# Performance work log

Measured on AMD Instinct MI355X. Metric: run time of the kernel, lower is better.

Reference implementation:

```python
import jax, jax.numpy as jnp
import numpy as np

N_NODES = 20000
N_EDGES = 320000
D_FEAT = 256
BATCH_SIZE = 4096


def setup_inputs() -> dict:
    key = jax.random.key(0)
    k1, k2 = jax.random.split(key)
    x = jax.random.normal(k1, (N_NODES, D_FEAT), dtype=jnp.float32)
    edge_index = jax.random.randint(k2, (2, N_EDGES), 0, N_NODES, dtype=jnp.int64)
    return {"x": x, "edge_index": edge_index, "batch_size": BATCH_SIZE}


def reference(x, edge_index, batch_size):
    # SparseTensor.from_edge_index: row = edge_index[0], col = edge_index[1].
    # gcn_norm(adj, add_self_loops=False): deg[r] = row-sum (edge count per row),
    # value(r, c) = deg[r]^-0.5 * deg[c]^-0.5.
    # adj_norm.t().matmul(x): out[c] = sum_{edges (r,c)} value * x[r].
    n = x.shape[0]
    src = edge_index[0]
    dst = edge_index[1]
    deg = jax.ops.segment_sum(jnp.ones_like(src, dtype=x.dtype), src, num_segments=n)
    deg_inv_sqrt = jnp.where(deg > 0, jax.lax.rsqrt(jnp.maximum(deg, 1.0)), 0.0)
    w = deg_inv_sqrt[src] * deg_inv_sqrt[dst]  # [E]
    # Weighted gather-scatter SpMM: [E, D] gathered rows -> scatter-add to dst.
    x_neighbors_norm = jax.ops.segment_sum(x[src] * w[:, None], dst, num_segments=n)
    node_labels = jnp.concatenate([x, x_neighbors_norm], axis=-1)  # [N, 2D]
    return node_labels[:batch_size]
```

## Files before the change

kernel.cpp:

```cpp
#include <hip/hip_runtime.h>

#define D_FEAT 256
#define CAP 96

__global__ __launch_bounds__(256) void edges_kernel(
        const int* __restrict__ src, const int* __restrict__ dst,
        int n_edges, int batch,
        int* __restrict__ degi, int* __restrict__ cursor,
        int* __restrict__ novf, int* __restrict__ buckets,
        long long* __restrict__ ovf) {
    int t = blockIdx.x * blockDim.x + threadIdx.x;
    int e = t * 4;
    if (e >= n_edges) return;

    int s[4], d[4];
    int rem = n_edges - e;
    if (rem >= 4) {
        int4 s4 = *(const int4*)(src + e);
        int4 d4 = *(const int4*)(dst + e);
        s[0] = s4.x; s[1] = s4.y; s[2] = s4.z; s[3] = s4.w;
        d[0] = d4.x; d[1] = d4.y; d[2] = d4.z; d[3] = d4.w;
    } else {
        for (int j = 0; j < 4; ++j) {
            s[j] = (j < rem) ? src[e + j] : 0;
            d[j] = (j < rem) ? dst[e + j] : 0x7fffffff;
        }
    }

#pragma unroll
    for (int j = 0; j < 4; ++j) {
        if (j < rem) atomicAdd(&degi[s[j]], 1);
        if (d[j] < batch) {
            int pos = atomicAdd(&cursor[d[j]], 1);
            if (pos < CAP) {
                buckets[(size_t)d[j] * CAP + pos] = s[j];
            } else {
                int op = atomicAdd(novf, 1);
                ovf[op] = ((long long)s[j] << 32) | (unsigned)d[j];
            }
        }
    }
}

__global__ __launch_bounds__(256) void aggregate_kernel(
        const float* __restrict__ x, const int* __restrict__ degi,
        const int* __restrict__ cursor, const int* __restrict__ buckets,
        int batch, float* __restrict__ out) {
    int gtid = blockIdx.x * blockDim.x + threadIdx.x;
    int r    = gtid >> 6;
    int lane = gtid & 63;
    if (r >= batch) return;

    int cnt = cursor[r];
    if (cnt > CAP) cnt = CAP;
    int dr = degi[r];
    float disr = (dr > 0) ? rsqrtf((float)dr) : 0.0f;
    const int* bk = buckets + (size_t)r * CAP;

    float4 acc = make_float4(0.f, 0.f, 0.f, 0.f);
    int i = 0;
    for (; i + 4 <= cnt; i += 4) {
        int s0 = bk[i], s1 = bk[i + 1], s2 = bk[i + 2], s3 = bk[i + 3];
        int g0 = degi[s0], g1 = degi[s1], g2 = degi[s2], g3 = degi[s3];
        float4 v0 = ((const float4*)(x + (size_t)s0 * D_FEAT))[lane];
        float4 v1 = ((const float4*)(x + (size_t)s1 * D_FEAT))[lane];
        float4 v2 = ((const float4*)(x + (size_t)s2 * D_FEAT))[lane];
        float4 v3 = ((const float4*)(x + (size_t)s3 * D_FEAT))[lane];
        float w0 = disr * rsqrtf((float)g0);
        float w1 = disr * rsqrtf((float)g1);
        float w2 = disr * rsqrtf((float)g2);
        float w3 = disr * rsqrtf((float)g3);
        acc.x += w0 * v0.x + w1 * v1.x + w2 * v2.x + w3 * v3.x;
        acc.y += w0 * v0.y + w1 * v1.y + w2 * v2.y + w3 * v3.y;
        acc.z += w0 * v0.z + w1 * v1.z + w2 * v2.z + w3 * v3.z;
        acc.w += w0 * v0.w + w1 * v1.w + w2 * v2.w + w3 * v3.w;
    }
    for (; i < cnt; ++i) {
        int s0 = bk[i];
        int g0 = degi[s0];
        float4 v0 = ((const float4*)(x + (size_t)s0 * D_FEAT))[lane];
        float w0 = disr * rsqrtf((float)g0);
        acc.x += w0 * v0.x; acc.y += w0 * v0.y;
        acc.z += w0 * v0.z; acc.w += w0 * v0.w;
    }

    float4 xv = ((const float4*)(x + (size_t)r * D_FEAT))[lane];
    float4* orow = (float4*)(out + (size_t)r * (2 * D_FEAT));
    orow[lane]      = xv;
    orow[64 + lane] = acc;
}

__global__ __launch_bounds__(256) void fixup_kernel(
        const float* __restrict__ x, const int* __restrict__ degi,
        const int* __restrict__ novf, const long long* __restrict__ ovf,
        float* __restrict__ out) {
    int n = *novf;
    int gtid = blockIdx.x * blockDim.x + threadIdx.x;
    int w    = gtid >> 6;
    int lane = gtid & 63;
    int nw   = (gridDim.x * blockDim.x) >> 6;
    for (int e = w; e < n; e += nw) {
        long long p = ovf[e];
        int d = (int)(p & 0xffffffff);
        int s = (int)(p >> 32);
        int gr = degi[d];
        float wgt = rsqrtf((float)degi[s]) *
                    ((gr > 0) ? rsqrtf((float)gr) : 0.0f);
        float4 v = ((const float4*)(x + (size_t)s * D_FEAT))[lane];
        float* o = out + (size_t)d * (2 * D_FEAT) + D_FEAT + lane * 4;
        unsafeAtomicAdd(o + 0, wgt * v.x);
        unsafeAtomicAdd(o + 1, wgt * v.y);
        unsafeAtomicAdd(o + 2, wgt * v.z);
        unsafeAtomicAdd(o + 3, wgt * v.w);
    }
}

__global__ void fb_deg_count(const int* __restrict__ src, int n_edges,
                             float* __restrict__ deg) {
    int e = blockIdx.x * blockDim.x + threadIdx.x;
    if (e < n_edges) unsafeAtomicAdd(&deg[src[e]], 1.0f);
}
__global__ void fb_deg_inv_sqrt(float* __restrict__ deg, int n_nodes) {
    int i = blockIdx.x * blockDim.x + threadIdx.x;
    if (i < n_nodes) { float d = deg[i]; deg[i] = (d > 0.f) ? rsqrtf(d) : 0.f; }
}
__global__ void fb_init_out(const float* __restrict__ x, float* __restrict__ out,
                            int batch) {
    int idx = blockIdx.x * blockDim.x + threadIdx.x;
    int row = idx >> 7, j = idx & 127;
    if (row < batch) {
        float4 v = (j < 64) ? ((const float4*)x)[row * 64 + j]
                            : make_float4(0.f, 0.f, 0.f, 0.f);
        ((float4*)out)[idx] = v;
    }
}
__global__ void fb_edge_scatter(const float* __restrict__ x,
                                const int* __restrict__ src,
                                const int* __restrict__ dst,
                                const float* __restrict__ dis,
                                int n_edges, int batch, float* __restrict__ out) {
    int gtid = blockIdx.x * blockDim.x + threadIdx.x;
    int e = gtid >> 6, lane = gtid & 63;
    if (e >= n_edges) return;
    int d = dst[e];
    if (d >= batch) return;
    int s = src[e];
    float w = dis[s] * dis[d];
    float4 v = ((const float4*)(x + (size_t)s * D_FEAT))[lane];
    float* o = out + (size_t)d * (2 * D_FEAT) + D_FEAT + lane * 4;
    unsafeAtomicAdd(o + 0, w * v.x);
    unsafeAtomicAdd(o + 1, w * v.y);
    unsafeAtomicAdd(o + 2, w * v.z);
    unsafeAtomicAdd(o + 3, w * v.w);
}

extern "C" void kernel_launch(void* const* d_in, const int* in_sizes, int n_in,
                              void* d_out, int out_size, void* d_ws, size_t ws_size,
                              hipStream_t stream) {
    const float* x  = (const float*)d_in[0];
    const int*   ei = (const int*)d_in[1];

    const int n_nodes = in_sizes[0] / D_FEAT;
    const int n_edges = in_sizes[1] / 2;
    const int batch   = out_size / (2 * D_FEAT);

    const int* src = ei;
    const int* dst = ei + n_edges;
    float* out = (float*)d_out;

    size_t need = ((size_t)n_nodes + batch + 1 + (size_t)batch * CAP) * 4
                + (size_t)n_edges * 8;

    if (ws_size >= need) {
        int*       degi    = (int*)d_ws;
        int*       cursor  = degi + n_nodes;
        int*       novf    = cursor + batch;
        int*       buckets = novf + 1;
        long long* ovf     = (long long*)(buckets + (size_t)batch * CAP);

        hipMemsetAsync(degi, 0, (size_t)(n_nodes + batch + 1) * 4, stream);

        int et = (n_edges + 3) / 4;
        edges_kernel<<<(et + 255) / 256, 256, 0, stream>>>(
            src, dst, n_edges, batch, degi, cursor, novf, buckets, ovf);

        long long th = (long long)batch * 64;
        aggregate_kernel<<<(int)((th + 255) / 256), 256, 0, stream>>>(
            x, degi, cursor, buckets, batch, out);

        fixup_kernel<<<64, 256, 0, stream>>>(x, degi, novf, ovf, out);
    } else {
        float* deg = (float*)d_ws;
        hipMemsetAsync(deg, 0, (size_t)n_nodes * sizeof(float), stream);
        fb_deg_count<<<(n_edges + 255) / 256, 256, 0, stream>>>(src, n_edges, deg);
        fb_deg_inv_sqrt<<<(n_nodes + 255) / 256, 256, 0, stream>>>(deg, n_nodes);
        fb_init_out<<<(batch * 128 + 255) / 256, 256, 0, stream>>>(x, out, batch);
        long long th = (long long)n_edges * 64;
        fb_edge_scatter<<<(int)((th + 255) / 256), 256, 0, stream>>>(
            x, src, dst, deg, n_edges, batch, out);
    }
}
```

Baseline: 99.90 us.

## Fuse memset, edge bucketing and aggregation into one cooperative kernel

Replaces the memset plus three kernel launches with a single cooperative-groups kernel. The phases (zeroing, edge bucketing with atomics, per-row aggregation) are separated by grid.sync() calls. Overflow edges are now folded in by each row scanning the whole overflow list instead of a separate atomic fixup kernel. This removes launch and inter-kernel gaps, but it caps the grid at the number of resident blocks and adds per-row work proportional to the overflow count. It also adds host-side attribute and occupancy queries on every call.

```diff
diff --git a/kernel.cpp b/kernel.cpp
--- a/kernel.cpp
+++ b/kernel.cpp
@@ -1,7 +1,117 @@
 #include <hip/hip_runtime.h>
+#include <hip/hip_cooperative_groups.h>
+
+namespace cg = cooperative_groups;
 
 #define D_FEAT 256
 #define CAP 96
+
+__global__ __launch_bounds__(256, 4) void fused_kernel(
+        const float* __restrict__ x,
+        const int* __restrict__ src, const int* __restrict__ dst,
+        int n_nodes, int n_edges, int batch,
+        int* __restrict__ degi, int* __restrict__ cursor,
+        int* __restrict__ novf, int* __restrict__ buckets,
+        long long* __restrict__ ovf,
+        float* __restrict__ out) {
+    cg::grid_group grid = cg::this_grid();
+    const int tid    = blockIdx.x * blockDim.x + threadIdx.x;
+    const int stride = gridDim.x * blockDim.x;
+
+    const int nzero = n_nodes + batch + 1;
+    for (int i = tid; i < nzero; i += stride) degi[i] = 0;
+
+    grid.sync();
+
+    const int nquad = (n_edges + 3) / 4;
+    for (int q = tid; q < nquad; q += stride) {
+        int e = q * 4;
+        int rem = n_edges - e;
+        int s[4], d[4];
+        if (rem >= 4) {
+            int4 s4 = *(const int4*)(src + e);
+            int4 d4 = *(const int4*)(dst + e);
+            s[0] = s4.x; s[1] = s4.y; s[2] = s4.z; s[3] = s4.w;
+            d[0] = d4.x; d[1] = d4.y; d[2] = d4.z; d[3] = d4.w;
+            rem = 4;
+        } else {
+            for (int j = 0; j < 4; ++j) {
+                s[j] = (j < rem) ? src[e + j] : 0;
+                d[j] = (j < rem) ? dst[e + j] : 0x7fffffff;
+            }
+        }
+#pragma unroll
+        for (int j = 0; j < 4; ++j) {
+            if (j < rem) atomicAdd(&degi[s[j]], 1);
+            if (d[j] < batch) {
+                int pos = atomicAdd(&cursor[d[j]], 1);
+                if (pos < CAP) {
+                    buckets[(size_t)d[j] * CAP + pos] = s[j];
+                } else {
+                    int op = atomicAdd(novf, 1);
+                    ovf[op] = ((long long)s[j] << 32) | (unsigned)d[j];
+                }
+            }
+        }
+    }
+
+    grid.sync();
+
+    const int lane   = tid & 63;
+    const int nwaves = stride >> 6;
+    const int n_ovf  = *novf;
+
+    for (int r = tid >> 6; r < batch; r += nwaves) {
+        int cnt = cursor[r];
+        if (cnt > CAP) cnt = CAP;
+        int dr = degi[r];
+        float disr = (dr > 0) ? rsqrtf((float)dr) : 0.0f;
+        const int* bk = buckets + (size_t)r * CAP;
+
+        float4 acc = make_float4(0.f, 0.f, 0.f, 0.f);
+        int i = 0;
+        for (; i + 4 <= cnt; i += 4) {
+            int s0 = bk[i], s1 = bk[i + 1], s2 = bk[i + 2], s3 = bk[i + 3];
+            int g0 = degi[s0], g1 = degi[s1], g2 = degi[s2], g3 = degi[s3];
+            float4 v0 = ((const float4*)(x + (size_t)s0 * D_FEAT))[lane];
+            float4 v1 = ((const float4*)(x + (size_t)s1 * D_FEAT))[lane];
+            float4 v2 = ((const float4*)(x + (size_t)s2 * D_FEAT))[lane];
+            float4 v3 = ((const float4*)(x + (size_t)s3 * D_FEAT))[lane];
+            float w0 = disr * rsqrtf((float)g0);
+            float w1 = disr * rsqrtf((float)g1);
+            float w2 = disr * rsqrtf((float)g2);
+            float w3 = disr * rsqrtf((float)g3);
+            acc.x += w0 * v0.x + w1 * v1.x + w2 * v2.x + w3 * v3.x;
+            acc.y += w0 * v0.y + w1 * v1.y + w2 * v2.y + w3 * v3.y;
+            acc.z += w0 * v0.z + w1 * v1.z + w2 * v2.z + w3 * v3.z;
+            acc.w += w0 * v0.w + w1 * v1.w + w2 * v2.w + w3 * v3.w;
+        }
+        for (; i < cnt; ++i) {
+            int s0 = bk[i];
+            int g0 = degi[s0];
+            float4 v0 = ((const float4*)(x + (size_t)s0 * D_FEAT))[lane];
+            float w0 = disr * rsqrtf((float)g0);
+            acc.x += w0 * v0.x; acc.y += w0 * v0.y;
+            acc.z += w0 * v0.z; acc.w += w0 * v0.w;
+        }
+        for (int k = 0; k < n_ovf; ++k) {
+            long long p = ovf[k];
+            int d = (int)(p & 0xffffffff);
+            if (d == r) {
+                int s0 = (int)(p >> 32);
+                float w0 = disr * rsqrtf((float)degi[s0]);
+                float4 v0 = ((const float4*)(x + (size_t)s0 * D_FEAT))[lane];
+                acc.x += w0 * v0.x; acc.y += w0 * v0.y;
+                acc.z += w0 * v0.z; acc.w += w0 * v0.w;
+            }
+        }
+
+        float4 xv = ((const float4*)(x + (size_t)r * D_FEAT))[lane];
+        float4* orow = (float4*)(out + (size_t)r * (2 * D_FEAT));
+        orow[lane]      = xv;
+        orow[64 + lane] = acc;
+    }
+}
 
 __global__ __launch_bounds__(256) void edges_kernel(
         const int* __restrict__ src, const int* __restrict__ dst,
@@ -12,7 +122,6 @@
     int t = blockIdx.x * blockDim.x + threadIdx.x;
     int e = t * 4;
     if (e >= n_edges) return;
-
     int s[4], d[4];
     int rem = n_edges - e;
     if (rem >= 4) {
@@ -20,21 +129,20 @@
         int4 d4 = *(const int4*)(dst + e);
         s[0] = s4.x; s[1] = s4.y; s[2] = s4.z; s[3] = s4.w;
         d[0] = d4.x; d[1] = d4.y; d[2] = d4.z; d[3] = d4.w;
+        rem = 4;
     } else {
         for (int j = 0; j < 4; ++j) {
             s[j] = (j < rem) ? src[e + j] : 0;
             d[j] = (j < rem) ? dst[e + j] : 0x7fffffff;
         }
     }
-
 #pragma unroll
     for (int j = 0; j < 4; ++j) {
         if (j < rem) atomicAdd(&degi[s[j]], 1);
         if (d[j] < batch) {
             int pos = atomicAdd(&cursor[d[j]], 1);
-            if (pos < CAP) {
-                buckets[(size_t)d[j] * CAP + pos] = s[j];
-            } else {
+            if (pos < CAP) buckets[(size_t)d[j] * CAP + pos] = s[j];
+            else {
                 int op = atomicAdd(novf, 1);
                 ovf[op] = ((long long)s[j] << 32) | (unsigned)d[j];
             }
@@ -50,13 +158,11 @@
     int r    = gtid >> 6;
     int lane = gtid & 63;
     if (r >= batch) return;
-
     int cnt = cursor[r];
     if (cnt > CAP) cnt = CAP;
     int dr = degi[r];
     float disr = (dr > 0) ? rsqrtf((float)dr) : 0.0f;
     const int* bk = buckets + (size_t)r * CAP;
-
     float4 acc = make_float4(0.f, 0.f, 0.f, 0.f);
     int i = 0;
     for (; i + 4 <= cnt; i += 4) {
@@ -83,7 +189,6 @@
         acc.x += w0 * v0.x; acc.y += w0 * v0.y;
         acc.z += w0 * v0.z; acc.w += w0 * v0.w;
     }
-
     float4 xv = ((const float4*)(x + (size_t)r * D_FEAT))[lane];
     float4* orow = (float4*)(out + (size_t)r * (2 * D_FEAT));
     orow[lane]      = xv;
@@ -96,16 +201,14 @@
         float* __restrict__ out) {
     int n = *novf;
     int gtid = blockIdx.x * blockDim.x + threadIdx.x;
-    int w    = gtid >> 6;
-    int lane = gtid & 63;
-    int nw   = (gridDim.x * blockDim.x) >> 6;
+    int w = gtid >> 6, lane = gtid & 63;
+    int nw = (gridDim.x * blockDim.x) >> 6;
     for (int e = w; e < n; e += nw) {
         long long p = ovf[e];
         int d = (int)(p & 0xffffffff);
         int s = (int)(p >> 32);
         int gr = degi[d];
-        float wgt = rsqrtf((float)degi[s]) *
-                    ((gr > 0) ? rsqrtf((float)gr) : 0.0f);
+        float wgt = rsqrtf((float)degi[s]) * ((gr > 0) ? rsqrtf((float)gr) : 0.0f);
         float4 v = ((const float4*)(x + (size_t)s * D_FEAT))[lane];
         float* o = out + (size_t)d * (2 * D_FEAT) + D_FEAT + lane * 4;
         unsafeAtomicAdd(o + 0, wgt * v.x);
@@ -178,17 +281,38 @@
         int*       buckets = novf + 1;
         long long* ovf     = (long long*)(buckets + (size_t)batch * CAP);
 
-        hipMemsetAsync(degi, 0, (size_t)(n_nodes + batch + 1) * 4, stream);
-
-        int et = (n_edges + 3) / 4;
-        edges_kernel<<<(et + 255) / 256, 256, 0, stream>>>(
-            src, dst, n_edges, batch, degi, cursor, novf, buckets, ovf);
-
-        long long th = (long long)batch * 64;
-        aggregate_kernel<<<(int)((th + 255) / 256), 256, 0, stream>>>(
-            x, degi, cursor, buckets, batch, out);
-
-        fixup_kernel<<<64, 256, 0, stream>>>(x, degi, novf, ovf, out);
+        int coop = 0;
+        hipDeviceGetAttribute(&coop, hipDeviceAttributeCooperativeLaunch, 0);
+
+        int want_blocks = (batch * 64 + 255) / 256;
+        int launched = 0;
+        if (coop) {
+            int perCU = 0, nCU = 0;
+            hipOccupancyMaxActiveBlocksPerMultiprocessor(
+                &perCU, (const void*)fused_kernel, 256, 0);
+            hipDeviceGetAttribute(&nCU, hipDeviceAttributeMultiprocessorCount, 0);
+            int maxb = perCU * nCU;
+            int nb = (want_blocks < maxb) ? want_blocks : maxb;
+            if (nb > 0) {
+                void* args[] = { (void*)&x, (void*)&src, (void*)&dst,
+                                 (void*)&n_nodes, (void*)&n_edges, (void*)&batch,
+                                 (void*)&degi, (void*)&cursor, (void*)&novf,
+                                 (void*)&buckets, (void*)&ovf, (void*)&out };
+                hipError_t err = hipLaunchCooperativeKernel(
+                    (const void*)fused_kernel, dim3(nb), dim3(256), args, 0, stream);
+                if (err == hipSuccess) launched = 1;
+            }
+        }
+        if (!launched) {
+            hipMemsetAsync(degi, 0, (size_t)(n_nodes + batch + 1) * 4, stream);
+            int et = (n_edges + 3) / 4;
+            edges_kernel<<<(et + 255) / 256, 256, 0, stream>>>(
+                src, dst, n_edges, batch, degi, cursor, novf, buckets, ovf);
+            long long th = (long long)batch * 64;
+            aggregate_kernel<<<(int)((th + 255) / 256), 256, 0, stream>>>(
+                x, degi, cursor, buckets, batch, out);
+            fixup_kernel<<<64, 256, 0, stream>>>(x, degi, novf, ovf, out);
+        }
     } else {
         float* deg = (float*)d_ws;
         hipMemsetAsync(deg, 0, (size_t)n_nodes * sizeof(float), stream);
```

Result: slower. 259.2 us (+159.5%).
